# Kernel tuning notes

Measured on AMD Instinct MI355X. Metric: run time of the kernel, lower is better.

Reference implementation:

```python
import jax, jax.numpy as jnp
import numpy as np
from jax import lax

B, T, C, H, W, SV = 1, 12, 10, 256, 256, 3
LAMBDA = 0.05
ITERS = 10


def _to_c(x):
    return lax.complex(x[..., 0], x[..., 1])


def _to_r(x):
    return jnp.stack([jnp.real(x), jnp.imag(x)], axis=-1)


def fft_2d_img(x):
    # torch: fftshift(ifft2(ifftshift(x)))  (backward-norm ifft, same as numpy/jax)
    ax = (-2, -1)
    return jnp.fft.fftshift(jnp.fft.ifft2(jnp.fft.ifftshift(x, axes=ax), axes=ax), axes=ax)


def ifft_2d_img(x):
    ax = (-2, -1)
    return jnp.fft.ifftshift(jnp.fft.fft2(jnp.fft.fftshift(x, axes=ax), axes=ax), axes=ax)


def setup_inputs() -> dict:
    key = jax.random.key(0)
    k0, k1, k2, k3, k4 = jax.random.split(key, 5)
    y = jax.random.normal(k0, (B, T, C, H, W, 2), jnp.float32)
    model_out = jax.random.normal(k1, (B, SV, H, W, 2), jnp.float32)
    sens = jax.random.normal(k2, (B, 1, C, H, W, 2), jnp.float32)
    time_basis = jax.random.normal(k3, (B, T, SV, 2), jnp.float32)
    mask = (jax.random.uniform(k4, (B, T, 1, H, W)) > 0.5).astype(jnp.float32)
    return dict(y=y, model_out=model_out, sens=sens, time_basis=time_basis, mask=mask)


def _adjoint(kspace, sens):
    # kspace: [b,t,c,h,w], sens: [b,1,c,h,w] -> [b,t,h,w]
    img = ifft_2d_img(kspace)
    return jnp.sum(jnp.conj(sens) * img, axis=2)


def _forward_model(data, sens, mask):
    # data: [b,t,h,w] -> masked k-space [b,t,c,h,w]
    coil = sens * data[:, :, None, :, :]
    return mask * fft_2d_img(coil)


def _system_R(x, sens, L, mask):
    # x: [b,sv,h,w]; L: [b,t,sv]
    b, sv, h, w = x.shape
    expanded = jnp.einsum('bts,bsp->btp', L, x.reshape(b, sv, h * w)).reshape(b, L.shape[1], h, w)
    masked_k = _forward_model(expanded, sens, mask)
    comb = _adjoint(masked_k, sens)  # [b,t,h,w]
    fin = jnp.einsum('bts,btp->bsp', jnp.conj(L), comb.reshape(b, L.shape[1], h * w))
    return fin.reshape(b, sv, h, w) + LAMBDA * x


def _cg_solve(A, b_vec):
    z = jnp.zeros_like(b_vec)
    r = b_vec
    p = r
    rs = jnp.vdot(r, r)

    def body(i, state):
        z, r, p, rs = state
        Ap = A(p)
        alpha = rs / jnp.vdot(p, Ap)
        z = z + alpha * p
        r = r - alpha * Ap
        rs_new = jnp.vdot(r, r)
        p = r + (rs_new / rs) * p
        return (z, r, p, rs_new)

    z, _, _, _ = lax.fori_loop(0, ITERS, body, (z, r, p, rs))
    return z


def reference(y, model_out, sens, time_basis, mask):
    yc = _to_c(y)            # [b,t,c,h,w] complex64
    sc = _to_c(sens)         # [b,1,c,h,w]
    mo = _to_c(model_out)    # [b,sv,h,w]
    L = _to_c(time_basis)    # [b,t,sv]
    b, t, c, h, w = yc.shape
    sv = L.shape[-1]

    ah_y = _adjoint(yc, sc)  # [b,t,h,w]
    b_vec = jnp.einsum('bts,btp->bsp', jnp.conj(L), ah_y.reshape(b, t, h * w)).reshape(b, sv, h, w)
    b_vec = b_vec + LAMBDA * mo

    A = lambda x: _system_R(x, sc, L, mask)
    z = _cg_solve(A, b_vec)  # [b,sv,h,w] complex
    return _to_r(z)          # [b,sv,h,w,2] float32
```

## Files before the change

### kernel.cpp

```cpp
#include <hip/hip_runtime.h>
#include <math.h>

#define HW 65536
#define NC 10
#define NT 12
#define LAMBDA_F 0.05f
#define PI_F 3.14159265358979323846f
#define SWZ(i) ((i) ^ ((i) >> 4))

__device__ __forceinline__ float2 cadd(float2 a, float2 b){ return make_float2(a.x+b.x, a.y+b.y); }
__device__ __forceinline__ float2 csub(float2 a, float2 b){ return make_float2(a.x-b.x, a.y-b.y); }
__device__ __forceinline__ float2 cmul(float2 a, float2 b){ return make_float2(a.x*b.x-a.y*b.y, a.x*b.y+a.y*b.x); }
__device__ __forceinline__ float2 cmulj(float2 a, float2 b){ return make_float2(a.x*b.x+a.y*b.y, a.x*b.y-a.y*b.x); }
__device__ __forceinline__ float2 cscale(float2 a, float s){ return make_float2(a.x*s, a.y*s); }

template<int SIGN>
__device__ __forceinline__ void radix4_nt(float2& a0, float2& a1, float2& a2, float2& a3){
  float2 t0=cadd(a0,a2), t1=csub(a0,a2), t2=cadd(a1,a3), t3=csub(a1,a3);
  float2 t3r;
  if constexpr (SIGN < 0) t3r = make_float2(t3.y, -t3.x); else t3r = make_float2(-t3.y, t3.x);
  a0=cadd(t0,t2); a1=cadd(t1,t3r); a2=csub(t0,t2); a3=csub(t1,t3r);
}

template<int SIGN>
__device__ __forceinline__ void radix4_tw(float2& a0, float2& a1, float2& a2, float2& a3, float2 w){
  if constexpr (SIGN > 0) w.y = -w.y;
  float2 w2 = cmul(w, w);
  float2 w3 = cmul(w, w2);
  a1 = cmul(a1, w); a2 = cmul(a2, w2); a3 = cmul(a3, w3);
  radix4_nt<SIGN>(a0, a1, a2, a3);
}

__device__ __forceinline__ float2 twf(int e){
  float s, c;
  __sincosf(-2.0f*PI_F*(float)e*(1.0f/256.0f), &s, &c);
  return make_float2(c, s);
}

template<int SIGN>
__device__ __forceinline__ void fft256(float2* b, int j,
                                       float2 wA, float2 wB, float2 wC,
                                       float2& x0, float2& x1, float2& x2, float2& x3){
  radix4_nt<SIGN>(x0,x1,x2,x3);
  b[SWZ(4*j)]=x0; b[SWZ(4*j+1)]=x1; b[SWZ(4*j+2)]=x2; b[SWZ(4*j+3)]=x3;
  x0=b[SWZ(j)]; x1=b[SWZ(j+64)]; x2=b[SWZ(j+128)]; x3=b[SWZ(j+192)];
  radix4_tw<SIGN>(x0,x1,x2,x3, wA);
  { int i=((j>>2)<<4)+(j&3); b[SWZ(i)]=x0; b[SWZ(i+4)]=x1; b[SWZ(i+8)]=x2; b[SWZ(i+12)]=x3; }
  x0=b[SWZ(j)]; x1=b[SWZ(j+64)]; x2=b[SWZ(j+128)]; x3=b[SWZ(j+192)];
  radix4_tw<SIGN>(x0,x1,x2,x3, wB);
  { int i=((j>>4)<<6)+(j&15); b[SWZ(i)]=x0; b[SWZ(i+16)]=x1; b[SWZ(i+32)]=x2; b[SWZ(i+48)]=x3; }
  x0=b[SWZ(j)]; x1=b[SWZ(j+64)]; x2=b[SWZ(j+128)]; x3=b[SWZ(j+192)];
  radix4_tw<SIGN>(x0,x1,x2,x3, wC);
}

template<int SIGN>
__device__ __forceinline__ void fft256x2(float2* bA, float2* bB, int j,
    float2 wA, float2 wB, float2 wC,
    float2& a0, float2& a1, float2& a2, float2& a3,
    float2& b0, float2& b1, float2& b2, float2& b3){
  radix4_nt<SIGN>(a0,a1,a2,a3); radix4_nt<SIGN>(b0,b1,b2,b3);
  bA[SWZ(4*j)]=a0; bA[SWZ(4*j+1)]=a1; bA[SWZ(4*j+2)]=a2; bA[SWZ(4*j+3)]=a3;
  bB[SWZ(4*j)]=b0; bB[SWZ(4*j+1)]=b1; bB[SWZ(4*j+2)]=b2; bB[SWZ(4*j+3)]=b3;
  a0=bA[SWZ(j)]; a1=bA[SWZ(j+64)]; a2=bA[SWZ(j+128)]; a3=bA[SWZ(j+192)];
  b0=bB[SWZ(j)]; b1=bB[SWZ(j+64)]; b2=bB[SWZ(j+128)]; b3=bB[SWZ(j+192)];
  radix4_tw<SIGN>(a0,a1,a2,a3, wA); radix4_tw<SIGN>(b0,b1,b2,b3, wA);
  { int i=((j>>2)<<4)+(j&3);
    bA[SWZ(i)]=a0; bA[SWZ(i+4)]=a1; bA[SWZ(i+8)]=a2; bA[SWZ(i+12)]=a3;
    bB[SWZ(i)]=b0; bB[SWZ(i+4)]=b1; bB[SWZ(i+8)]=b2; bB[SWZ(i+12)]=b3; }
  a0=bA[SWZ(j)]; a1=bA[SWZ(j+64)]; a2=bA[SWZ(j+128)]; a3=bA[SWZ(j+192)];
  b0=bB[SWZ(j)]; b1=bB[SWZ(j+64)]; b2=bB[SWZ(j+128)]; b3=bB[SWZ(j+192)];
  radix4_tw<SIGN>(a0,a1,a2,a3, wB); radix4_tw<SIGN>(b0,b1,b2,b3, wB);
  { int i=((j>>4)<<6)+(j&15);
    bA[SWZ(i)]=a0; bA[SWZ(i+16)]=a1; bA[SWZ(i+32)]=a2; bA[SWZ(i+48)]=a3;
    bB[SWZ(i)]=b0; bB[SWZ(i+16)]=b1; bB[SWZ(i+32)]=b2; bB[SWZ(i+48)]=b3; }
  a0=bA[SWZ(j)]; a1=bA[SWZ(j+64)]; a2=bA[SWZ(j+128)]; a3=bA[SWZ(j+192)];
  b0=bB[SWZ(j)]; b1=bB[SWZ(j+64)]; b2=bB[SWZ(j+128)]; b3=bB[SWZ(j+192)];
  radix4_tw<SIGN>(a0,a1,a2,a3, wC); radix4_tw<SIGN>(b0,b1,b2,b3, wC);
}

__device__ __forceinline__ void cg_chain(const float* __restrict__ scal,
                                         float f0, float f1, float f2, float f3, float f4,
                                         float rs0, int it,
                                         float& a_re, float& a_im, float& beta){
  float rs = rs0; a_re = 0.f; a_im = 0.f; beta = 0.f;
  for (int k = 0; k < it; k++){
    float pr, pi, rr_, ri_, aa;
    if (k == it-1){ pr=f0; pi=f1; rr_=f2; ri_=f3; aa=f4; }
    else { pr=scal[8+8*k+0]; pi=scal[8+8*k+1]; rr_=scal[8+8*k+2];
           ri_=scal[8+8*k+3]; aa=scal[8+8*k+4]; }
    float den = pr*pr + pi*pi;
    a_re =  rs*pr/den;
    a_im = -rs*pi/den;
    float re_ = a_re*rr_ - a_im*ri_;
    float rs_next = rs - 2.0f*re_ + (a_re*a_re + a_im*a_im)*aa;
    beta = rs_next/rs;
    rs = rs_next;
  }
}

__global__ __launch_bounds__(256) void k_setup(const float* __restrict__ mask,
                                               const float2* __restrict__ Lt,
                                               const float2* __restrict__ y,
                                               float* __restrict__ W9,
                                               float2* __restrict__ bufB,
                                               float* __restrict__ scal,
                                               float* __restrict__ part){
  int tid = threadIdx.x;
  int u = blockIdx.x;
  if (u == 0){
    if (tid < 128) scal[tid] = 0.0f;
    for (int i = tid; i < 6144; i += 256) part[i] = 0.0f;
  }
  if (u < 256){
    int kx = u, ky = tid;
    int mx = (kx + 128) & 255, my = (ky + 128) & 255;
    float d0=0.f,d1=0.f,d2=0.f;
    float2 o01=make_float2(0,0), o02=make_float2(0,0), o12=make_float2(0,0);
    for (int t = 0; t < NT; t++){
      float m = mask[t*HW + my*256 + mx];
      float2 l0 = Lt[t*3+0], l1 = Lt[t*3+1], l2 = Lt[t*3+2];
      d0 += m*(l0.x*l0.x + l0.y*l0.y);
      d1 += m*(l1.x*l1.x + l1.y*l1.y);
      d2 += m*(l2.x*l2.x + l2.y*l2.y);
      o01 = cadd(o01, cscale(cmulj(l0,l1), m));
      o02 = cadd(o02, cscale(cmulj(l0,l2), m));
      o12 = cadd(o12, cscale(cmulj(l1,l2), m));
    }
    const float nrm = 1.0f/65536.0f;
    int idx = kx*256 + ky;
    W9[idx]      = d0*nrm;  W9[idx+HW]   = d1*nrm;  W9[idx+2*HW] = d2*nrm;
    W9[idx+3*HW] = o01.x*nrm; W9[idx+4*HW] = o01.y*nrm;
    W9[idx+5*HW] = o02.x*nrm; W9[idx+6*HW] = o02.y*nrm;
    W9[idx+7*HW] = o12.x*nrm; W9[idx+8*HW] = o12.y*nrm;
  } else {
    int idx = (u-256)*256 + tid;
    int c = idx >> 16, pix = idx & (HW-1);
    int xx = pix & 255, yy2 = pix >> 8;
    float sg = ((xx + yy2) & 1) ? -1.0f : 1.0f;
    float2 a0=make_float2(0,0), a1=make_float2(0,0), a2=make_float2(0,0);
    for (int t = 0; t < NT; t++){
      float2 yv = y[((size_t)(t*NC + c))*HW + pix];
      a0 = cadd(a0, cmulj(Lt[t*3+0], yv));
      a1 = cadd(a1, cmulj(Lt[t*3+1], yv));
      a2 = cadd(a2, cmulj(Lt[t*3+2], yv));
    }
    bufB[((size_t)(c*3+0))*HW + pix] = cscale(a0, sg);
    bufB[((size_t)(c*3+1))*HW + pix] = cscale(a1, sg);
    bufB[((size_t)(c*3+2))*HW + pix] = cscale(a2, sg);
  }
}

__global__ __launch_bounds__(512) void k_rows_plain(const float2* __restrict__ src,
                                                    float2* __restrict__ dst){
  __shared__ float2 tile[8][256];
  int tid = threadIdx.x, g = tid >> 6, j = tid & 63;
  float2 wA = twf((j&3)<<4), wB = twf((j&15)<<2), wC = twf(j);
  int pl = blockIdx.y, ri = blockIdx.x;
  int row = ri*8 + g;
  const float2* sr = src + (size_t)pl*HW + row*256;
  float2 x0=sr[j], x1=sr[j+64], x2=sr[j+128], x3=sr[j+192];
  fft256<-1>(tile[g], j, wA,wB,wC, x0,x1,x2,x3);
  tile[g][j]=x0; tile[g][j+64]=x1; tile[g][j+128]=x2; tile[g][j+192]=x3;
  __syncthreads();
  float2* dT = dst + (size_t)pl*HW;
  int yo2 = (tid&3)*2, kxo = tid>>2;
  #pragma unroll
  for (int kb = 0; kb < 2; kb++){
    int kx = kb*128 + kxo;
    float2 a = tile[yo2][kx], b = tile[yo2+1][kx];
    *(float4*)(dT + (size_t)kx*256 + ri*8 + yo2) = make_float4(a.x,a.y,b.x,b.y);
  }
}

__global__ __launch_bounds__(512) void k_cols_plain(const float2* __restrict__ src,
                                                    float2* __restrict__ dst){
  __shared__ float2 tile[8][256];
  int tid = threadIdx.x, g = tid >> 6, j = tid & 63;
  float2 wA = twf((j&3)<<4), wB = twf((j&15)<<2), wC = twf(j);
  int pl = blockIdx.y, kg = blockIdx.x;
  int kx = kg*8 + g;
  const float2* col = src + (size_t)pl*HW + (size_t)kx*256;
  float2 x0=col[j], x1=col[j+64], x2=col[j+128], x3=col[j+192];
  fft256<-1>(tile[g], j, wA,wB,wC, x0,x1,x2,x3);
  tile[g][j]=x0; tile[g][j+64]=x1; tile[g][j+128]=x2; tile[g][j+192]=x3;
  __syncthreads();
  float2* d = dst + (size_t)pl*HW;
  int kxo2 = (tid&3)*2, yy = tid>>2;
  #pragma unroll
  for (int yb = 0; yb < 2; yb++){
    int yc = yb*128 + yy;
    float2 a = tile[kxo2][yc], b = tile[kxo2+1][yc];
    *(float4*)(d + (size_t)yc*256 + kg*8 + kxo2) = make_float4(a.x,a.y,b.x,b.y);
  }
}

__global__ __launch_bounds__(256) void k_compute_b(const float2* __restrict__ A,
                                                   const float2* __restrict__ sens,
                                                   const float2* __restrict__ mo,
                                                   float2* __restrict__ p,
                                                   float2* __restrict__ r,
                                                   float2* __restrict__ z,
                                                   float* __restrict__ part){
  __shared__ float red[4];
  int idx = blockIdx.x*256 + threadIdx.x;
  int s = idx >> 16, pix = idx & (HW-1);
  int xx = pix & 255, yy = pix >> 8;
  float sg = ((xx + yy) & 1) ? -1.0f : 1.0f;
  float2 accv = make_float2(0,0);
  for (int c = 0; c < NC; c++)
    accv = cadd(accv, cmulj(sens[(size_t)c*HW + pix], A[((size_t)(c*3+s))*HW + pix]));
  float2 b = cadd(cscale(accv, sg), cscale(mo[idx], LAMBDA_F));
  p[idx] = b; r[idx] = b; z[idx] = make_float2(0,0);
  float partv = b.x*b.x + b.y*b.y;
  for (int off = 32; off; off >>= 1) partv += __shfl_down(partv, off);
  int j = threadIdx.x & 63, w = threadIdx.x >> 6;
  if (j == 0) red[w] = partv;
  __syncthreads();
  if (threadIdx.x == 0) part[5*1024 + blockIdx.x] = red[0]+red[1]+red[2]+red[3];
}

__global__ __launch_bounds__(256) void k_rows_op(const float2* __restrict__ rprev,
                                                 const float2* __restrict__ pprev,
                                                 const float2* __restrict__ Apb,
                                                 float2* __restrict__ pout,
                                                 float2* __restrict__ rout,
                                                 float2* __restrict__ z,
                                                 const float2* __restrict__ sens,
                                                 float2* __restrict__ dst,
                                                 float* __restrict__ scal,
                                                 const float* __restrict__ part,
                                                 int iter){
  __shared__ float2 tile[8][256];
  __shared__ float red6[4][6];
  int tid = threadIdx.x, g = tid >> 6, j = tid & 63;
  float2 wA = twf((j&3)<<4), wB = twf((j&15)<<2), wC = twf(j);
  int pl = blockIdx.y, ri = blockIdx.x;
  int c = pl/3, sp = pl - 3*c;
  const float2* Sp = sens + (size_t)c*HW;

  float a_re=0.f, a_im=0.f, beta=0.f;
  if (iter > 0){
    float v[6];
    #pragma unroll
    for (int q = 0; q < 6; q++){
      float x = part[q*1024+tid] + part[q*1024+tid+256]
              + part[q*1024+tid+512] + part[q*1024+tid+768];
      for (int off = 32; off; off >>= 1) x += __shfl_down(x, off);
      v[q] = x;
    }
    if (j == 0){
      #pragma unroll
      for (int q = 0; q < 6; q++) red6[g][q] = v[q];
    }
    __syncthreads();
    float f0 = red6[0][0]+red6[1][0]+red6[2][0]+red6[3][0];
    float f1 = red6[0][1]+red6[1][1]+red6[2][1]+red6[3][1];
    float f2 = red6[0][2]+red6[1][2]+red6[2][2]+red6[3][2];
    float f3 = red6[0][3]+red6[1][3]+red6[2][3]+red6[3][3];
    float f4 = red6[0][4]+red6[1][4]+red6[2][4]+red6[3][4];
    float rs0 = (iter == 1) ? (red6[0][5]+red6[1][5]+red6[2][5]+red6[3][5]) : scal[0];
    cg_chain(scal, f0,f1,f2,f3,f4, rs0, iter, a_re, a_im, beta);
    if (blockIdx.x == 0 && blockIdx.y == 0 && tid == 0){
      scal[8+8*(iter-1)+0]=f0; scal[8+8*(iter-1)+1]=f1; scal[8+8*(iter-1)+2]=f2;
      scal[8+8*(iter-1)+3]=f3; scal[8+8*(iter-1)+4]=f4;
      if (iter == 1) scal[0] = rs0;
    }
  }

  int row0 = ri*8 + g*2, row1 = row0 + 1;
  int baseA = row0*256, baseB = row1*256;
  size_t pbA = (size_t)sp*HW + baseA, pbB = (size_t)sp*HW + baseB;
  float2 pvA[4], pvB[4];
  if (iter == 0){
    #pragma unroll
    for (int q = 0; q < 4; q++){
      pvA[q] = pprev[pbA + j + 64*q];
      pvB[q] = pprev[pbB + j + 64*q];
    }
  } else {
    #pragma unroll
    for (int q = 0; q < 4; q++){
      int x = j + 64*q;
      float2 peA = pprev[pbA+x], reA = rprev[pbA+x], aeA = Apb[pbA+x];
      float2 peB = pprev[pbB+x], reB = rprev[pbB+x], aeB = Apb[pbB+x];
      float2 rnA = make_float2(reA.x - (a_re*aeA.x - a_im*aeA.y),
                               reA.y - (a_re*aeA.y + a_im*aeA.x));
      float2 rnB = make_float2(reB.x - (a_re*aeB.x - a_im*aeB.y),
                               reB.y - (a_re*aeB.y + a_im*aeB.x));
      pvA[q] = make_float2(rnA.x + beta*peA.x, rnA.y + beta*peA.y);
      pvB[q] = make_float2(rnB.x + beta*peB.x, rnB.y + beta*peB.y);
      if (c == 0){
        rout[pbA+x] = rnA;  rout[pbB+x] = rnB;
        pout[pbA+x] = pvA[q]; pout[pbB+x] = pvB[q];
        float2 zA = z[pbA+x], zB = z[pbB+x];
        z[pbA+x] = make_float2(zA.x + a_re*peA.x - a_im*peA.y,
                               zA.y + a_re*peA.y + a_im*peA.x);
        z[pbB+x] = make_float2(zB.x + a_re*peB.x - a_im*peB.y,
                               zB.y + a_re*peB.y + a_im*peB.x);
      }
    }
  }
  float2 xA0 = cmul(Sp[baseA+j],     pvA[0]);
  float2 xA1 = cmul(Sp[baseA+j+64],  pvA[1]);
  float2 xA2 = cmul(Sp[baseA+j+128], pvA[2]);
  float2 xA3 = cmul(Sp[baseA+j+192], pvA[3]);
  float2 xB0 = cmul(Sp[baseB+j],     pvB[0]);
  float2 xB1 = cmul(Sp[baseB+j+64],  pvB[1]);
  float2 xB2 = cmul(Sp[baseB+j+128], pvB[2]);
  float2 xB3 = cmul(Sp[baseB+j+192], pvB[3]);
  fft256x2<1>(tile[g*2], tile[g*2+1], j, wA,wB,wC, xA0,xA1,xA2,xA3, xB0,xB1,xB2,xB3);
  tile[g*2][j]=xA0; tile[g*2][j+64]=xA1; tile[g*2][j+128]=xA2; tile[g*2][j+192]=xA3;
  tile[g*2+1][j]=xB0; tile[g*2+1][j+64]=xB1; tile[g*2+1][j+128]=xB2; tile[g*2+1][j+192]=xB3;
  __syncthreads();
  float2* dT = dst + (size_t)pl*HW;
  int yo2 = (tid&3)*2, kxo = tid>>2;
  #pragma unroll
  for (int kb = 0; kb < 4; kb++){
    int kx = kb*64 + kxo;
    float2 a = tile[yo2][kx], b = tile[yo2+1][kx];
    *(float4*)(dT + (size_t)kx*256 + ri*8 + yo2) = make_float4(a.x,a.y,b.x,b.y);
  }
}

__global__ __launch_bounds__(384) void k_cols_W(const float2* __restrict__ src,
                                                float2* __restrict__ dst,
                                                const float* __restrict__ W9){
  __shared__ float2 tile[12][256];
  int tid = threadIdx.x, w = tid >> 6, j = tid & 63;
  float2 wA = twf((j&3)<<4), wB = twf((j&15)<<2), wC = twf(j);
  int kg = blockIdx.x, c = blockIdx.y;
  int s = w >> 1, kxp = w & 1;
  int kxl0 = kxp*2, kxl1 = kxl0+1;
  int kx0 = kg*4 + kxl0, kx1 = kg*4 + kxl1;
  {
    const float2* colA = src + ((size_t)(c*3+s))*HW + (size_t)kx0*256;
    const float2* colB = src + ((size_t)(c*3+s))*HW + (size_t)kx1*256;
    float2 a0=colA[j], a1=colA[j+64], a2=colA[j+128], a3=colA[j+192];
    float2 b0=colB[j], b1=colB[j+64], b2=colB[j+128], b3=colB[j+192];
    fft256x2<1>(tile[s*4+kxl0], tile[s*4+kxl1], j, wA,wB,wC, a0,a1,a2,a3, b0,b1,b2,b3);
    tile[s*4+kxl0][j]=a0; tile[s*4+kxl0][j+64]=a1; tile[s*4+kxl0][j+128]=a2; tile[s*4+kxl0][j+192]=a3;
    tile[s*4+kxl1][j]=b0; tile[s*4+kxl1][j+64]=b1; tile[s*4+kxl1][j+128]=b2; tile[s*4+kxl1][j+192]=b3;
  }
  __syncthreads();
  float2 UA[4], UB[4];
  #pragma unroll
  for (int q = 0; q < 4; q++){
    int k = j + 64*q;
    {
      int wi = kx0*256 + k;
      float2 v0 = tile[0+kxl0][k], v1 = tile[4+kxl0][k], v2 = tile[8+kxl0][k];
      if (s == 0){
        float d0 = W9[wi];
        float2 o01 = make_float2(W9[wi+3*HW], W9[wi+4*HW]);
        float2 o02 = make_float2(W9[wi+5*HW], W9[wi+6*HW]);
        UA[q] = cadd(cadd(cscale(v0,d0), cmul(o01,v1)), cmul(o02,v2));
      } else if (s == 1){
        float d1 = W9[wi+HW];
        float2 o01 = make_float2(W9[wi+3*HW], W9[wi+4*HW]);
        float2 o12 = make_float2(W9[wi+7*HW], W9[wi+8*HW]);
        UA[q] = cadd(cadd(cmulj(o01,v0), cscale(v1,d1)), cmul(o12,v2));
      } else {
        float d2 = W9[wi+2*HW];
        float2 o02 = make_float2(W9[wi+5*HW], W9[wi+6*HW]);
        float2 o12 = make_float2(W9[wi+7*HW], W9[wi+8*HW]);
        UA[q] = cadd(cadd(cmulj(o02,v0), cmulj(o12,v1)), cscale(v2,d2));
      }
    }
    {
      int wi = kx1*256 + k;
      float2 v0 = tile[0+kxl1][k], v1 = tile[4+kxl1][k], v2 = tile[8+kxl1][k];
      if (s == 0){
        float d0 = W9[wi];
        float2 o01 = make_float2(W9[wi+3*HW], W9[wi+4*HW]);
        float2 o02 = make_float2(W9[wi+5*HW], W9[wi+6*HW]);
        UB[q] = cadd(cadd(cscale(v0,d0), cmul(o01,v1)), cmul(o02,v2));
      } else if (s == 1){
        float d1 = W9[wi+HW];
        float2 o01 = make_float2(W9[wi+3*HW], W9[wi+4*HW]);
        float2 o12 = make_float2(W9[wi+7*HW], W9[wi+8*HW]);
        UB[q] = cadd(cadd(cmulj(o01,v0), cscale(v1,d1)), cmul(o12,v2));
      } else {
        float d2 = W9[wi+2*HW];
        float2 o02 = make_float2(W9[wi+5*HW], W9[wi+6*HW]);
        float2 o12 = make_float2(W9[wi+7*HW], W9[wi+8*HW]);
        UB[q] = cadd(cadd(cmulj(o02,v0), cmulj(o12,v1)), cscale(v2,d2));
      }
    }
  }
  __syncthreads();
  {
    float2 a0=UA[0], a1=UA[1], a2=UA[2], a3=UA[3];
    float2 b0=UB[0], b1=UB[1], b2=UB[2], b3=UB[3];
    fft256x2<-1>(tile[s*4+kxl0], tile[s*4+kxl1], j, wA,wB,wC, a0,a1,a2,a3, b0,b1,b2,b3);
    tile[s*4+kxl0][j]=a0; tile[s*4+kxl0][j+64]=a1; tile[s*4+kxl0][j+128]=a2; tile[s*4+kxl0][j+192]=a3;
    tile[s*4+kxl1][j]=b0; tile[s*4+kxl1][j+64]=b1; tile[s*4+kxl1][j+128]=b2; tile[s*4+kxl1][j+192]=b3;
  }
  __syncthreads();
  #pragma unroll
  for (int yb = 0; yb < 4; yb++){
    int flat = yb*384 + tid;
    int s_out = flat >> 9;
    int rem = flat & 511;
    int kxo2 = (rem >> 8) << 1;
    int yc = rem & 255;
    float2 a = tile[s_out*4+kxo2][yc], b = tile[s_out*4+kxo2+1][yc];
    float2* d = dst + ((size_t)(c*3+s_out))*HW;
    *(float4*)(d + (size_t)yc*256 + kg*4 + kxo2) = make_float4(a.x,a.y,b.x,b.y);
  }
}

__global__ __launch_bounds__(320) void k_rows_acc(const float2* __restrict__ Bp,
                                                  const float2* __restrict__ sens,
                                                  const float2* __restrict__ p,
                                                  const float2* __restrict__ r,
                                                  float2* __restrict__ Ap,
                                                  float* __restrict__ part){
  __shared__ float2 scratch[10][256];
  __shared__ float red5[4][5];
  int tid = threadIdx.x, w = tid >> 6, j = tid & 63;
  float2 wA = twf((j&3)<<4), wB = twf((j&15)<<2), wC = twf(j);
  int row = blockIdx.x, s = blockIdx.y;
  {
    int c0 = 2*w, c1 = 2*w+1;
    const float2* srcA = Bp + ((size_t)(c0*3+s))*HW + row*256;
    const float2* srcB = Bp + ((size_t)(c1*3+s))*HW + row*256;
    float2 a0=srcA[j], a1=srcA[j+64], a2=srcA[j+128], a3=srcA[j+192];
    float2 b0=srcB[j], b1=srcB[j+64], b2=srcB[j+128], b3=srcB[j+192];
    fft256x2<-1>(scratch[c0], scratch[c1], j, wA,wB,wC, a0,a1,a2,a3, b0,b1,b2,b3);
    const float2* ScA = sens + (size_t)c0*HW + row*256;
    const float2* ScB = sens + (size_t)c1*HW + row*256;
    scratch[c0][j]     = cmulj(ScA[j],     a0);
    scratch[c0][j+64]  = cmulj(ScA[j+64],  a1);
    scratch[c0][j+128] = cmulj(ScA[j+128], a2);
    scratch[c0][j+192] = cmulj(ScA[j+192], a3);
    scratch[c1][j]     = cmulj(ScB[j],     b0);
    scratch[c1][j+64]  = cmulj(ScB[j+64],  b1);
    scratch[c1][j+128] = cmulj(ScB[j+128], b2);
    scratch[c1][j+192] = cmulj(ScB[j+192], b3);
  }
  __syncthreads();
  if (tid < 256){
    int k = tid;
    float2 a = make_float2(0,0);
    #pragma unroll
    for (int c = 0; c < NC; c++) a = cadd(a, scratch[c][k]);
    size_t ob = (size_t)s*HW + row*256 + k;
    float2 pv = p[ob];
    float2 ap = cadd(a, cscale(pv, LAMBDA_F));
    Ap[ob] = ap;
    float2 rv = r[ob];
    float s0 = pv.x*ap.x + pv.y*ap.y;
    float s1 = pv.x*ap.y - pv.y*ap.x;
    float s2 = rv.x*ap.x + rv.y*ap.y;
    float s3 = rv.x*ap.y - rv.y*ap.x;
    float s4 = ap.x*ap.x + ap.y*ap.y;
    for (int off = 32; off; off >>= 1){
      s0 += __shfl_down(s0, off); s1 += __shfl_down(s1, off);
      s2 += __shfl_down(s2, off); s3 += __shfl_down(s3, off);
      s4 += __shfl_down(s4, off);
    }
    if (j == 0){ red5[w][0]=s0; red5[w][1]=s1; red5[w][2]=s2; red5[w][3]=s3; red5[w][4]=s4; }
  }
  __syncthreads();
  if (tid == 0){
    int bflat = blockIdx.y*256 + blockIdx.x;
    #pragma unroll
    for (int q = 0; q < 5; q++)
      part[q*1024 + bflat] = red5[0][q]+red5[1][q]+red5[2][q]+red5[3][q];
  }
}

__global__ __launch_bounds__(256) void k_zfin(float2* __restrict__ z,
                                              const float2* __restrict__ p9,
                                              const float* __restrict__ scal,
                                              const float* __restrict__ part){
  __shared__ float red5[4][5];
  int tid = threadIdx.x, g = tid >> 6, j = tid & 63;
  float v[5];
  #pragma unroll
  for (int q = 0; q < 5; q++){
    float x = part[q*1024+tid] + part[q*1024+tid+256]
            + part[q*1024+tid+512] + part[q*1024+tid+768];
    for (int off = 32; off; off >>= 1) x += __shfl_down(x, off);
    v[q] = x;
  }
  if (j == 0){
    #pragma unroll
    for (int q = 0; q < 5; q++) red5[g][q] = v[q];
  }
  __syncthreads();
  float f0 = red5[0][0]+red5[1][0]+red5[2][0]+red5[3][0];
  float f1 = red5[0][1]+red5[1][1]+red5[2][1]+red5[3][1];
  float f2 = red5[0][2]+red5[1][2]+red5[2][2]+red5[3][2];
  float f3 = red5[0][3]+red5[1][3]+red5[2][3]+red5[3][3];
  float f4 = red5[0][4]+red5[1][4]+red5[2][4]+red5[3][4];
  float a_re, a_im, beta;
  cg_chain(scal, f0,f1,f2,f3,f4, scal[0], 10, a_re, a_im, beta);
  int idx = blockIdx.x*256 + tid;
  float2 pe = p9[idx], ze = z[idx];
  z[idx] = make_float2(ze.x + a_re*pe.x - a_im*pe.y,
                       ze.y + a_re*pe.y + a_im*pe.x);
}

extern "C" void kernel_launch(void* const* d_in, const int* in_sizes, int n_in,
                              void* d_out, int out_size, void* d_ws, size_t ws_size,
                              hipStream_t stream){
  const float2* y    = (const float2*)d_in[0];
  const float2* mo   = (const float2*)d_in[1];
  const float2* sens = (const float2*)d_in[2];
  const float2* Lt   = (const float2*)d_in[3];
  const float*  mask = (const float*)d_in[4];

  float* w = (float*)d_ws;
  float*  scal = w;
  float*  part = w + 128;
  float*  W9   = w + 128 + 6144;
  float2* bufA = (float2*)(W9 + 9*HW);
  float2* bufB = bufA + (size_t)30*HW;
  float2* p0   = bufB + (size_t)30*HW;
  float2* p1   = p0 + (size_t)3*HW;
  float2* r0   = p1 + (size_t)3*HW;
  float2* r1   = r0 + (size_t)3*HW;
  float2* Ap   = r1 + (size_t)3*HW;
  float2* z    = (float2*)d_out;

  k_setup<<<2816, 256, 0, stream>>>(mask, Lt, y, W9, bufB, scal, part);
  k_rows_plain<<<dim3(32, 30), 512, 0, stream>>>(bufB, bufA);
  k_cols_plain<<<dim3(32, 30), 512, 0, stream>>>(bufA, bufB);
  k_compute_b<<<768, 256, 0, stream>>>(bufB, sens, mo, p0, r0, z, part);

  for (int it = 0; it < 10; it++){
    float2* pprev = (it == 0) ? p0 : ((it & 1) ? p0 : p1);
    float2* rprev = (it == 0) ? r0 : ((it & 1) ? r0 : r1);
    float2* pw = (it & 1) ? p1 : p0;
    float2* rw = (it & 1) ? r1 : r0;
    k_rows_op<<<dim3(32, 30), 256, 0, stream>>>(rprev, pprev, Ap, pw, rw, z, sens, bufA, scal, part, it);
    k_cols_W<<<dim3(64, 10), 384, 0, stream>>>(bufA, bufB, W9);
    k_rows_acc<<<dim3(256, 3), 320, 0, stream>>>(bufB, sens, pw, rw, Ap, part);
  }
  k_zfin<<<768, 256, 0, stream>>>(z, p1, scal, part);
}
```

Measured before the change: 474.1 us.

## Restructure CG loop into two kernels per iteration using linearity of forward FFT

Reworks each CG iteration from three kernels into two. The column FFT of the search direction p is built from the FFT of r plus beta times the previous k-space direction (Kp), so only r needs a forward row FFT. The row adjoint FFT, coil sum, CG update and forward row FFT of the new residual are fused into one 640-thread kernel. The pAp inner product is computed in the k-space weighting stage, and alpha comes from a recurrence over the stored rs history. This cuts launches and a full pass over the 30-plane buffers per iteration, at the cost of an extra 30-plane Kp buffer that is read and written each iteration, and a different floating-point summation order.

After: 645.0 us. 36.1% more time.

```diff
diff --git a/kernel.cpp b/kernel.cpp
--- a/kernel.cpp
+++ b/kernel.cpp
@@ -7,6 +7,9 @@
 #define LAMBDA_F 0.05f
 #define PI_F 3.14159265358979323846f
 #define SWZ(i) ((i) ^ ((i) >> 4))
+#define ROW_RS(it)  (it)
+#define ROW_PAR(it) (16 + 2*(it))
+#define NPART_ROWS 36
 
 __device__ __forceinline__ float2 cadd(float2 a, float2 b){ return make_float2(a.x+b.x, a.y+b.y); }
 __device__ __forceinline__ float2 csub(float2 a, float2 b){ return make_float2(a.x-b.x, a.y-b.y); }
@@ -78,24 +81,22 @@
   radix4_tw<SIGN>(a0,a1,a2,a3, wC); radix4_tw<SIGN>(b0,b1,b2,b3, wC);
 }
 
-__device__ __forceinline__ void cg_chain(const float* __restrict__ scal,
-                                         float f0, float f1, float f2, float f3, float f4,
-                                         float rs0, int it,
-                                         float& a_re, float& a_im, float& beta){
-  float rs = rs0; a_re = 0.f; a_im = 0.f; beta = 0.f;
-  for (int k = 0; k < it; k++){
-    float pr, pi, rr_, ri_, aa;
-    if (k == it-1){ pr=f0; pi=f1; rr_=f2; ri_=f3; aa=f4; }
-    else { pr=scal[8+8*k+0]; pi=scal[8+8*k+1]; rr_=scal[8+8*k+2];
-           ri_=scal[8+8*k+3]; aa=scal[8+8*k+4]; }
-    float den = pr*pr + pi*pi;
-    a_re =  rs*pr/den;
-    a_im = -rs*pi/den;
-    float re_ = a_re*rr_ - a_im*ri_;
-    float rs_next = rs - 2.0f*re_ + (a_re*a_re + a_im*a_im)*aa;
-    beta = rs_next/rs;
-    rs = rs_next;
-  }
+__device__ __forceinline__ void cg_chain2(const float* __restrict__ scal, int n,
+                                          float parR, float parI,
+                                          float& a_re, float& a_im, float& beta){
+  float rs0 = scal[0];
+  float P2 = rs0, rs_km1 = rs0;
+  beta = 0.f;
+  for (int k = 1; k < n; k++){
+    float rsk = scal[k];
+    beta = rsk / rs_km1;
+    P2 = rsk + beta*beta*P2;
+    rs_km1 = rsk;
+  }
+  float pr = parR + LAMBDA_F*P2, pi = parI;
+  float den = pr*pr + pi*pi;
+  a_re =  rs_km1*pr/den;
+  a_im = -rs_km1*pi/den;
 }
 
 __global__ __launch_bounds__(256) void k_setup(const float* __restrict__ mask,
@@ -109,7 +110,7 @@
   int u = blockIdx.x;
   if (u == 0){
     if (tid < 128) scal[tid] = 0.0f;
-    for (int i = tid; i < 6144; i += 256) part[i] = 0.0f;
+    for (int i = tid; i < NPART_ROWS*1024; i += 256) part[i] = 0.0f;
   }
   if (u < 256){
     int kx = u, ky = tid;
@@ -197,7 +198,6 @@
 __global__ __launch_bounds__(256) void k_compute_b(const float2* __restrict__ A,
                                                    const float2* __restrict__ sens,
                                                    const float2* __restrict__ mo,
-                                                   float2* __restrict__ p,
                                                    float2* __restrict__ r,
                                                    float2* __restrict__ z,
                                                    float* __restrict__ part){
@@ -210,192 +210,257 @@
   for (int c = 0; c < NC; c++)
     accv = cadd(accv, cmulj(sens[(size_t)c*HW + pix], A[((size_t)(c*3+s))*HW + pix]));
   float2 b = cadd(cscale(accv, sg), cscale(mo[idx], LAMBDA_F));
-  p[idx] = b; r[idx] = b; z[idx] = make_float2(0,0);
+  r[idx] = b; z[idx] = make_float2(0,0);
   float partv = b.x*b.x + b.y*b.y;
   for (int off = 32; off; off >>= 1) partv += __shfl_down(partv, off);
   int j = threadIdx.x & 63, w = threadIdx.x >> 6;
   if (j == 0) red[w] = partv;
   __syncthreads();
-  if (threadIdx.x == 0) part[5*1024 + blockIdx.x] = red[0]+red[1]+red[2]+red[3];
-}
-
-__global__ __launch_bounds__(256) void k_rows_op(const float2* __restrict__ rprev,
-                                                 const float2* __restrict__ pprev,
-                                                 const float2* __restrict__ Apb,
-                                                 float2* __restrict__ pout,
-                                                 float2* __restrict__ rout,
-                                                 float2* __restrict__ z,
-                                                 const float2* __restrict__ sens,
-                                                 float2* __restrict__ dst,
-                                                 float* __restrict__ scal,
-                                                 const float* __restrict__ part,
-                                                 int iter){
-  __shared__ float2 tile[8][256];
-  __shared__ float red6[4][6];
-  int tid = threadIdx.x, g = tid >> 6, j = tid & 63;
+  if (threadIdx.x == 0) part[ROW_RS(0)*1024 + blockIdx.x] = red[0]+red[1]+red[2]+red[3];
+}
+
+template<int MODE>
+__global__ __launch_bounds__(640) void k_bigrow(const float2* __restrict__ bufB,
+                                                const float2* __restrict__ sens,
+                                                float2* __restrict__ rbuf,
+                                                float2* __restrict__ pbuf,
+                                                float2* __restrict__ zbuf,
+                                                float2* __restrict__ bufR,
+                                                const float* __restrict__ scal,
+                                                float* __restrict__ part, int iter){
+  __shared__ float2 scratch[10][256];
+  __shared__ float2 rnew_s[256];
+  __shared__ float redv[10];
+  __shared__ float sA[2];
+  int tid = threadIdx.x, w = tid >> 6, j = tid & 63;
   float2 wA = twf((j&3)<<4), wB = twf((j&15)<<2), wC = twf(j);
-  int pl = blockIdx.y, ri = blockIdx.x;
-  int c = pl/3, sp = pl - 3*c;
-  const float2* Sp = sens + (size_t)c*HW;
-
-  float a_re=0.f, a_im=0.f, beta=0.f;
-  if (iter > 0){
-    float v[6];
+  int row = blockIdx.x, s = blockIdx.y;
+
+  if constexpr (MODE == 1){
     #pragma unroll
-    for (int q = 0; q < 6; q++){
-      float x = part[q*1024+tid] + part[q*1024+tid+256]
-              + part[q*1024+tid+512] + part[q*1024+tid+768];
-      for (int off = 32; off; off >>= 1) x += __shfl_down(x, off);
-      v[q] = x;
-    }
-    if (j == 0){
+    for (int q = 0; q < 2; q++){
+      const float* P = part + (ROW_PAR(iter-1)+q)*1024;
+      float v = P[tid] + ((tid < 384) ? P[tid+640] : 0.f);
+      for (int off = 32; off; off >>= 1) v += __shfl_down(v, off);
+      if (j == 0) redv[w] = v;
+      __syncthreads();
+      if (tid == 0){
+        float t = 0.f;
+        #pragma unroll
+        for (int k = 0; k < 10; k++) t += redv[k];
+        sA[q] = t;
+      }
+      __syncthreads();
+    }
+    float a_re, a_im, beta;
+    cg_chain2(scal, iter, sA[0], sA[1], a_re, a_im, beta);
+
+    {
+      int c = w;
+      const float2* src = bufB + ((size_t)(c*3+s))*HW + row*256;
+      float2 x0=src[j], x1=src[j+64], x2=src[j+128], x3=src[j+192];
+      fft256<-1>(scratch[c], j, wA,wB,wC, x0,x1,x2,x3);
+      const float2* Sc = sens + (size_t)c*HW + row*256;
+      scratch[c][j]     = cmulj(Sc[j],     x0);
+      scratch[c][j+64]  = cmulj(Sc[j+64],  x1);
+      scratch[c][j+128] = cmulj(Sc[j+128], x2);
+      scratch[c][j+192] = cmulj(Sc[j+192], x3);
+    }
+    __syncthreads();
+    if (tid < 256){
+      int k = tid;
+      float2 M = make_float2(0,0);
       #pragma unroll
-      for (int q = 0; q < 6; q++) red6[g][q] = v[q];
-    }
-    __syncthreads();
-    float f0 = red6[0][0]+red6[1][0]+red6[2][0]+red6[3][0];
-    float f1 = red6[0][1]+red6[1][1]+red6[2][1]+red6[3][1];
-    float f2 = red6[0][2]+red6[1][2]+red6[2][2]+red6[3][2];
-    float f3 = red6[0][3]+red6[1][3]+red6[2][3]+red6[3][3];
-    float f4 = red6[0][4]+red6[1][4]+red6[2][4]+red6[3][4];
-    float rs0 = (iter == 1) ? (red6[0][5]+red6[1][5]+red6[2][5]+red6[3][5]) : scal[0];
-    cg_chain(scal, f0,f1,f2,f3,f4, rs0, iter, a_re, a_im, beta);
-    if (blockIdx.x == 0 && blockIdx.y == 0 && tid == 0){
-      scal[8+8*(iter-1)+0]=f0; scal[8+8*(iter-1)+1]=f1; scal[8+8*(iter-1)+2]=f2;
-      scal[8+8*(iter-1)+3]=f3; scal[8+8*(iter-1)+4]=f4;
-      if (iter == 1) scal[0] = rs0;
-    }
-  }
-
-  int row0 = ri*8 + g*2, row1 = row0 + 1;
-  int baseA = row0*256, baseB = row1*256;
-  size_t pbA = (size_t)sp*HW + baseA, pbB = (size_t)sp*HW + baseB;
-  float2 pvA[4], pvB[4];
-  if (iter == 0){
-    #pragma unroll
-    for (int q = 0; q < 4; q++){
-      pvA[q] = pprev[pbA + j + 64*q];
-      pvB[q] = pprev[pbB + j + 64*q];
-    }
+      for (int c = 0; c < NC; c++) M = cadd(M, scratch[c][k]);
+      size_t ob = (size_t)s*HW + row*256 + k;
+      float2 rold = rbuf[ob];
+      float2 pcur;
+      if (iter == 1) pcur = rold;
+      else { float2 pold = pbuf[ob]; pcur = cadd(rold, cscale(pold, beta)); }
+      float2 Ap = cadd(M, cscale(pcur, LAMBDA_F));
+      float2 rnew = make_float2(rold.x - (a_re*Ap.x - a_im*Ap.y),
+                                rold.y - (a_re*Ap.y + a_im*Ap.x));
+      float2 zo = zbuf[ob];
+      zbuf[ob] = make_float2(zo.x + a_re*pcur.x - a_im*pcur.y,
+                             zo.y + a_re*pcur.y + a_im*pcur.x);
+      pbuf[ob] = pcur;
+      rbuf[ob] = rnew;
+      rnew_s[k] = rnew;
+      float pv2 = rnew.x*rnew.x + rnew.y*rnew.y;
+      for (int off = 32; off; off >>= 1) pv2 += __shfl_down(pv2, off);
+      if (j == 0) redv[w] = pv2;
+    }
+    __syncthreads();
+    if (tid == 0)
+      part[ROW_RS(iter)*1024 + s*256 + row] = redv[0]+redv[1]+redv[2]+redv[3];
   } else {
-    #pragma unroll
-    for (int q = 0; q < 4; q++){
-      int x = j + 64*q;
-      float2 peA = pprev[pbA+x], reA = rprev[pbA+x], aeA = Apb[pbA+x];
-      float2 peB = pprev[pbB+x], reB = rprev[pbB+x], aeB = Apb[pbB+x];
-      float2 rnA = make_float2(reA.x - (a_re*aeA.x - a_im*aeA.y),
-                               reA.y - (a_re*aeA.y + a_im*aeA.x));
-      float2 rnB = make_float2(reB.x - (a_re*aeB.x - a_im*aeB.y),
-                               reB.y - (a_re*aeB.y + a_im*aeB.x));
-      pvA[q] = make_float2(rnA.x + beta*peA.x, rnA.y + beta*peA.y);
-      pvB[q] = make_float2(rnB.x + beta*peB.x, rnB.y + beta*peB.y);
-      if (c == 0){
-        rout[pbA+x] = rnA;  rout[pbB+x] = rnB;
-        pout[pbA+x] = pvA[q]; pout[pbB+x] = pvB[q];
-        float2 zA = z[pbA+x], zB = z[pbB+x];
-        z[pbA+x] = make_float2(zA.x + a_re*peA.x - a_im*peA.y,
-                               zA.y + a_re*peA.y + a_im*peA.x);
-        z[pbB+x] = make_float2(zB.x + a_re*peB.x - a_im*peB.y,
-                               zB.y + a_re*peB.y + a_im*peB.x);
-      }
-    }
-  }
-  float2 xA0 = cmul(Sp[baseA+j],     pvA[0]);
-  float2 xA1 = cmul(Sp[baseA+j+64],  pvA[1]);
-  float2 xA2 = cmul(Sp[baseA+j+128], pvA[2]);
-  float2 xA3 = cmul(Sp[baseA+j+192], pvA[3]);
-  float2 xB0 = cmul(Sp[baseB+j],     pvB[0]);
-  float2 xB1 = cmul(Sp[baseB+j+64],  pvB[1]);
-  float2 xB2 = cmul(Sp[baseB+j+128], pvB[2]);
-  float2 xB3 = cmul(Sp[baseB+j+192], pvB[3]);
-  fft256x2<1>(tile[g*2], tile[g*2+1], j, wA,wB,wC, xA0,xA1,xA2,xA3, xB0,xB1,xB2,xB3);
-  tile[g*2][j]=xA0; tile[g*2][j+64]=xA1; tile[g*2][j+128]=xA2; tile[g*2][j+192]=xA3;
-  tile[g*2+1][j]=xB0; tile[g*2+1][j+64]=xB1; tile[g*2+1][j+128]=xB2; tile[g*2+1][j+192]=xB3;
-  __syncthreads();
-  float2* dT = dst + (size_t)pl*HW;
-  int yo2 = (tid&3)*2, kxo = tid>>2;
-  #pragma unroll
-  for (int kb = 0; kb < 4; kb++){
-    int kx = kb*64 + kxo;
-    float2 a = tile[yo2][kx], b = tile[yo2+1][kx];
-    *(float4*)(dT + (size_t)kx*256 + ri*8 + yo2) = make_float4(a.x,a.y,b.x,b.y);
-  }
-}
-
-__global__ __launch_bounds__(384) void k_cols_W(const float2* __restrict__ src,
-                                                float2* __restrict__ dst,
-                                                const float* __restrict__ W9){
-  __shared__ float2 tile[12][256];
+    if (tid < 256){
+      size_t ob = (size_t)s*HW + row*256 + tid;
+      rnew_s[tid] = rbuf[ob];
+    }
+    __syncthreads();
+  }
+
+  {
+    int c = w;
+    const float2* Sc = sens + (size_t)c*HW + row*256;
+    float2 x0 = cmul(Sc[j],     rnew_s[j]);
+    float2 x1 = cmul(Sc[j+64],  rnew_s[j+64]);
+    float2 x2 = cmul(Sc[j+128], rnew_s[j+128]);
+    float2 x3 = cmul(Sc[j+192], rnew_s[j+192]);
+    fft256<1>(scratch[c], j, wA,wB,wC, x0,x1,x2,x3);
+    float2* d = bufR + ((size_t)(c*3+s))*HW + row*256;
+    d[j]=x0; d[j+64]=x1; d[j+128]=x2; d[j+192]=x3;
+  }
+}
+
+__global__ __launch_bounds__(384) void k_colW(const float2* __restrict__ bufR,
+                                              float2* __restrict__ Kp,
+                                              float2* __restrict__ bufB,
+                                              const float* __restrict__ W9,
+                                              float* __restrict__ scal,
+                                              float* __restrict__ part, int iter){
+  __shared__ float2 T[12][256];
+  __shared__ float redv[6][2];
+  __shared__ float sB[1];
   int tid = threadIdx.x, w = tid >> 6, j = tid & 63;
   float2 wA = twf((j&3)<<4), wB = twf((j&15)<<2), wC = twf(j);
   int kg = blockIdx.x, c = blockIdx.y;
   int s = w >> 1, kxp = w & 1;
-  int kxl0 = kxp*2, kxl1 = kxl0+1;
+  int kxl0 = kxp*2, kxl1 = kxl0 + 1;
   int kx0 = kg*4 + kxl0, kx1 = kg*4 + kxl1;
+
+  float rs_it;
   {
-    const float2* colA = src + ((size_t)(c*3+s))*HW + (size_t)kx0*256;
-    const float2* colB = src + ((size_t)(c*3+s))*HW + (size_t)kx1*256;
-    float2 a0=colA[j], a1=colA[j+64], a2=colA[j+128], a3=colA[j+192];
-    float2 b0=colB[j], b1=colB[j+64], b2=colB[j+128], b3=colB[j+192];
-    fft256x2<1>(tile[s*4+kxl0], tile[s*4+kxl1], j, wA,wB,wC, a0,a1,a2,a3, b0,b1,b2,b3);
-    tile[s*4+kxl0][j]=a0; tile[s*4+kxl0][j+64]=a1; tile[s*4+kxl0][j+128]=a2; tile[s*4+kxl0][j+192]=a3;
-    tile[s*4+kxl1][j]=b0; tile[s*4+kxl1][j+64]=b1; tile[s*4+kxl1][j+128]=b2; tile[s*4+kxl1][j+192]=b3;
-  }
-  __syncthreads();
+    const float* P = part + ROW_RS(iter)*1024;
+    float v = P[tid] + P[tid+384] + ((tid < 256) ? P[tid+768] : 0.f);
+    for (int off = 32; off; off >>= 1) v += __shfl_down(v, off);
+    if (j == 0) redv[w][0] = v;
+    __syncthreads();
+    if (tid == 0){
+      float t = 0.f;
+      #pragma unroll
+      for (int k = 0; k < 6; k++) t += redv[k][0];
+      sB[0] = t;
+    }
+    __syncthreads();
+    rs_it = sB[0];
+  }
+  float beta = (iter == 0) ? 0.f : rs_it / scal[iter-1];
+  if (blockIdx.x == 0 && blockIdx.y == 0 && tid == 0) scal[iter] = rs_it;
+
+  #pragma unroll
+  for (int f = 0; f < 4; f++){
+    int idx = f*384 + tid;
+    int sp = idx >> 9, rem = idx & 511, rrow = rem >> 1, cp = rem & 1;
+    const float4* s4 = (const float4*)(bufR + ((size_t)(c*3+sp))*HW);
+    float4 v = s4[(size_t)rrow*128 + kg*2 + cp];
+    T[sp*4 + cp*2 + 0][rrow] = make_float2(v.x, v.y);
+    T[sp*4 + cp*2 + 1][rrow] = make_float2(v.z, v.w);
+  }
+  __syncthreads();
+
+  float2 a0=T[s*4+kxl0][j], a1=T[s*4+kxl0][j+64], a2=T[s*4+kxl0][j+128], a3=T[s*4+kxl0][j+192];
+  float2 b0=T[s*4+kxl1][j], b1=T[s*4+kxl1][j+64], b2=T[s*4+kxl1][j+128], b3=T[s*4+kxl1][j+192];
+  fft256x2<1>(T[s*4+kxl0], T[s*4+kxl1], j, wA,wB,wC, a0,a1,a2,a3, b0,b1,b2,b3);
+
+  float2* kpA = Kp + ((size_t)(c*3+s))*HW + (size_t)kx0*256;
+  float2* kpB = Kp + ((size_t)(c*3+s))*HW + (size_t)kx1*256;
+  if (iter > 0){
+    a0 = cadd(a0, cscale(kpA[j],     beta));
+    a1 = cadd(a1, cscale(kpA[j+64],  beta));
+    a2 = cadd(a2, cscale(kpA[j+128], beta));
+    a3 = cadd(a3, cscale(kpA[j+192], beta));
+    b0 = cadd(b0, cscale(kpB[j],     beta));
+    b1 = cadd(b1, cscale(kpB[j+64],  beta));
+    b2 = cadd(b2, cscale(kpB[j+128], beta));
+    b3 = cadd(b3, cscale(kpB[j+192], beta));
+  }
+  kpA[j]=a0; kpA[j+64]=a1; kpA[j+128]=a2; kpA[j+192]=a3;
+  kpB[j]=b0; kpB[j+64]=b1; kpB[j+128]=b2; kpB[j+192]=b3;
+  T[s*4+kxl0][j]=a0; T[s*4+kxl0][j+64]=a1; T[s*4+kxl0][j+128]=a2; T[s*4+kxl0][j+192]=a3;
+  T[s*4+kxl1][j]=b0; T[s*4+kxl1][j+64]=b1; T[s*4+kxl1][j+128]=b2; T[s*4+kxl1][j+192]=b3;
+  __syncthreads();
+
   float2 UA[4], UB[4];
+  float pr = 0.f, pim = 0.f;
   #pragma unroll
   for (int q = 0; q < 4; q++){
     int k = j + 64*q;
     {
       int wi = kx0*256 + k;
-      float2 v0 = tile[0+kxl0][k], v1 = tile[4+kxl0][k], v2 = tile[8+kxl0][k];
+      float2 v0 = T[0+kxl0][k], v1 = T[4+kxl0][k], v2 = T[8+kxl0][k];
+      float2 U;
       if (s == 0){
         float d0 = W9[wi];
         float2 o01 = make_float2(W9[wi+3*HW], W9[wi+4*HW]);
         float2 o02 = make_float2(W9[wi+5*HW], W9[wi+6*HW]);
-        UA[q] = cadd(cadd(cscale(v0,d0), cmul(o01,v1)), cmul(o02,v2));
+        U = cadd(cadd(cscale(v0,d0), cmul(o01,v1)), cmul(o02,v2));
       } else if (s == 1){
         float d1 = W9[wi+HW];
         float2 o01 = make_float2(W9[wi+3*HW], W9[wi+4*HW]);
         float2 o12 = make_float2(W9[wi+7*HW], W9[wi+8*HW]);
-        UA[q] = cadd(cadd(cmulj(o01,v0), cscale(v1,d1)), cmul(o12,v2));
+        U = cadd(cadd(cmulj(o01,v0), cscale(v1,d1)), cmul(o12,v2));
       } else {
         float d2 = W9[wi+2*HW];
         float2 o02 = make_float2(W9[wi+5*HW], W9[wi+6*HW]);
         float2 o12 = make_float2(W9[wi+7*HW], W9[wi+8*HW]);
-        UA[q] = cadd(cadd(cmulj(o02,v0), cmulj(o12,v1)), cscale(v2,d2));
+        U = cadd(cadd(cmulj(o02,v0), cmulj(o12,v1)), cscale(v2,d2));
       }
+      UA[q] = U;
+      float2 vs = (s==0) ? v0 : ((s==1) ? v1 : v2);
+      pr  += vs.x*U.x + vs.y*U.y;
+      pim += vs.x*U.y - vs.y*U.x;
     }
     {
       int wi = kx1*256 + k;
-      float2 v0 = tile[0+kxl1][k], v1 = tile[4+kxl1][k], v2 = tile[8+kxl1][k];
+      float2 v0 = T[0+kxl1][k], v1 = T[4+kxl1][k], v2 = T[8+kxl1][k];
+      float2 U;
       if (s == 0){
         float d0 = W9[wi];
         float2 o01 = make_float2(W9[wi+3*HW], W9[wi+4*HW]);
         float2 o02 = make_float2(W9[wi+5*HW], W9[wi+6*HW]);
-        UB[q] = cadd(cadd(cscale(v0,d0), cmul(o01,v1)), cmul(o02,v2));
+        U = cadd(cadd(cscale(v0,d0), cmul(o01,v1)), cmul(o02,v2));
       } else if (s == 1){
         float d1 = W9[wi+HW];
         float2 o01 = make_float2(W9[wi+3*HW], W9[wi+4*HW]);
         float2 o12 = make_float2(W9[wi+7*HW], W9[wi+8*HW]);
-        UB[q] = cadd(cadd(cmulj(o01,v0), cscale(v1,d1)), cmul(o12,v2));
+        U = cadd(cadd(cmulj(o01,v0), cscale(v1,d1)), cmul(o12,v2));
       } else {
         float d2 = W9[wi+2*HW];
         float2 o02 = make_float2(W9[wi+5*HW], W9[wi+6*HW]);
         float2 o12 = make_float2(W9[wi+7*HW], W9[wi+8*HW]);
-        UB[q] = cadd(cadd(cmulj(o02,v0), cmulj(o12,v1)), cscale(v2,d2));
+        U = cadd(cadd(cmulj(o02,v0), cmulj(o12,v1)), cscale(v2,d2));
       }
-    }
-  }
-  __syncthreads();
+      UB[q] = U;
+      float2 vs = (s==0) ? v0 : ((s==1) ? v1 : v2);
+      pr  += vs.x*U.x + vs.y*U.y;
+      pim += vs.x*U.y - vs.y*U.x;
+    }
+  }
+  __syncthreads();
+
   {
-    float2 a0=UA[0], a1=UA[1], a2=UA[2], a3=UA[3];
-    float2 b0=UB[0], b1=UB[1], b2=UB[2], b3=UB[3];
-    fft256x2<-1>(tile[s*4+kxl0], tile[s*4+kxl1], j, wA,wB,wC, a0,a1,a2,a3, b0,b1,b2,b3);
-    tile[s*4+kxl0][j]=a0; tile[s*4+kxl0][j+64]=a1; tile[s*4+kxl0][j+128]=a2; tile[s*4+kxl0][j+192]=a3;
-    tile[s*4+kxl1][j]=b0; tile[s*4+kxl1][j+64]=b1; tile[s*4+kxl1][j+128]=b2; tile[s*4+kxl1][j+192]=b3;
-  }
-  __syncthreads();
+    float2 c0=UA[0], c1=UA[1], c2=UA[2], c3=UA[3];
+    float2 d0=UB[0], d1=UB[1], d2=UB[2], d3=UB[3];
+    fft256x2<-1>(T[s*4+kxl0], T[s*4+kxl1], j, wA,wB,wC, c0,c1,c2,c3, d0,d1,d2,d3);
+    T[s*4+kxl0][j]=c0; T[s*4+kxl0][j+64]=c1; T[s*4+kxl0][j+128]=c2; T[s*4+kxl0][j+192]=c3;
+    T[s*4+kxl1][j]=d0; T[s*4+kxl1][j+64]=d1; T[s*4+kxl1][j+128]=d2; T[s*4+kxl1][j+192]=d3;
+  }
+  for (int off = 32; off; off >>= 1){
+    pr  += __shfl_down(pr, off);
+    pim += __shfl_down(pim, off);
+  }
+  if (j == 0){ redv[w][0] = pr; redv[w][1] = pim; }
+  __syncthreads();
+  if (tid == 0){
+    float tr = 0.f, ti = 0.f;
+    #pragma unroll
+    for (int k = 0; k < 6; k++){ tr += redv[k][0]; ti += redv[k][1]; }
+    int bflat = c*64 + kg;
+    part[ ROW_PAR(iter)   *1024 + bflat] = tr;
+    part[(ROW_PAR(iter)+1)*1024 + bflat] = ti;
+  }
   #pragma unroll
   for (int yb = 0; yb < 4; yb++){
     int flat = yb*384 + tid;
@@ -403,103 +468,38 @@
     int rem = flat & 511;
     int kxo2 = (rem >> 8) << 1;
     int yc = rem & 255;
-    float2 a = tile[s_out*4+kxo2][yc], b = tile[s_out*4+kxo2+1][yc];
-    float2* d = dst + ((size_t)(c*3+s_out))*HW;
+    float2 a = T[s_out*4+kxo2][yc], b = T[s_out*4+kxo2+1][yc];
+    float2* d = bufB + ((size_t)(c*3+s_out))*HW;
     *(float4*)(d + (size_t)yc*256 + kg*4 + kxo2) = make_float4(a.x,a.y,b.x,b.y);
   }
 }
 
-__global__ __launch_bounds__(320) void k_rows_acc(const float2* __restrict__ Bp,
-                                                  const float2* __restrict__ sens,
-                                                  const float2* __restrict__ p,
-                                                  const float2* __restrict__ r,
-                                                  float2* __restrict__ Ap,
-                                                  float* __restrict__ part){
-  __shared__ float2 scratch[10][256];
-  __shared__ float red5[4][5];
+__global__ __launch_bounds__(256) void k_final(float2* __restrict__ z,
+                                               const float2* __restrict__ rbuf,
+                                               const float2* __restrict__ pbuf,
+                                               const float* __restrict__ scal,
+                                               const float* __restrict__ part){
+  __shared__ float redv[4];
+  __shared__ float sA[2];
   int tid = threadIdx.x, w = tid >> 6, j = tid & 63;
-  float2 wA = twf((j&3)<<4), wB = twf((j&15)<<2), wC = twf(j);
-  int row = blockIdx.x, s = blockIdx.y;
-  {
-    int c0 = 2*w, c1 = 2*w+1;
-    const float2* srcA = Bp + ((size_t)(c0*3+s))*HW + row*256;
-    const float2* srcB = Bp + ((size_t)(c1*3+s))*HW + row*256;
-    float2 a0=srcA[j], a1=srcA[j+64], a2=srcA[j+128], a3=srcA[j+192];
-    float2 b0=srcB[j], b1=srcB[j+64], b2=srcB[j+128], b3=srcB[j+192];
-    fft256x2<-1>(scratch[c0], scratch[c1], j, wA,wB,wC, a0,a1,a2,a3, b0,b1,b2,b3);
-    const float2* ScA = sens + (size_t)c0*HW + row*256;
-    const float2* ScB = sens + (size_t)c1*HW + row*256;
-    scratch[c0][j]     = cmulj(ScA[j],     a0);
-    scratch[c0][j+64]  = cmulj(ScA[j+64],  a1);
-    scratch[c0][j+128] = cmulj(ScA[j+128], a2);
-    scratch[c0][j+192] = cmulj(ScA[j+192], a3);
-    scratch[c1][j]     = cmulj(ScB[j],     b0);
-    scratch[c1][j+64]  = cmulj(ScB[j+64],  b1);
-    scratch[c1][j+128] = cmulj(ScB[j+128], b2);
-    scratch[c1][j+192] = cmulj(ScB[j+192], b3);
-  }
-  __syncthreads();
-  if (tid < 256){
-    int k = tid;
-    float2 a = make_float2(0,0);
-    #pragma unroll
-    for (int c = 0; c < NC; c++) a = cadd(a, scratch[c][k]);
-    size_t ob = (size_t)s*HW + row*256 + k;
-    float2 pv = p[ob];
-    float2 ap = cadd(a, cscale(pv, LAMBDA_F));
-    Ap[ob] = ap;
-    float2 rv = r[ob];
-    float s0 = pv.x*ap.x + pv.y*ap.y;
-    float s1 = pv.x*ap.y - pv.y*ap.x;
-    float s2 = rv.x*ap.x + rv.y*ap.y;
-    float s3 = rv.x*ap.y - rv.y*ap.x;
-    float s4 = ap.x*ap.x + ap.y*ap.y;
-    for (int off = 32; off; off >>= 1){
-      s0 += __shfl_down(s0, off); s1 += __shfl_down(s1, off);
-      s2 += __shfl_down(s2, off); s3 += __shfl_down(s3, off);
-      s4 += __shfl_down(s4, off);
-    }
-    if (j == 0){ red5[w][0]=s0; red5[w][1]=s1; red5[w][2]=s2; red5[w][3]=s3; red5[w][4]=s4; }
-  }
-  __syncthreads();
-  if (tid == 0){
-    int bflat = blockIdx.y*256 + blockIdx.x;
-    #pragma unroll
-    for (int q = 0; q < 5; q++)
-      part[q*1024 + bflat] = red5[0][q]+red5[1][q]+red5[2][q]+red5[3][q];
-  }
-}
-
-__global__ __launch_bounds__(256) void k_zfin(float2* __restrict__ z,
-                                              const float2* __restrict__ p9,
-                                              const float* __restrict__ scal,
-                                              const float* __restrict__ part){
-  __shared__ float red5[4][5];
-  int tid = threadIdx.x, g = tid >> 6, j = tid & 63;
-  float v[5];
   #pragma unroll
-  for (int q = 0; q < 5; q++){
-    float x = part[q*1024+tid] + part[q*1024+tid+256]
-            + part[q*1024+tid+512] + part[q*1024+tid+768];
-    for (int off = 32; off; off >>= 1) x += __shfl_down(x, off);
-    v[q] = x;
-  }
-  if (j == 0){
-    #pragma unroll
-    for (int q = 0; q < 5; q++) red5[g][q] = v[q];
-  }
-  __syncthreads();
-  float f0 = red5[0][0]+red5[1][0]+red5[2][0]+red5[3][0];
-  float f1 = red5[0][1]+red5[1][1]+red5[2][1]+red5[3][1];
-  float f2 = red5[0][2]+red5[1][2]+red5[2][2]+red5[3][2];
-  float f3 = red5[0][3]+red5[1][3]+red5[2][3]+red5[3][3];
-  float f4 = red5[0][4]+red5[1][4]+red5[2][4]+red5[3][4];
+  for (int q = 0; q < 2; q++){
+    const float* P = part + (ROW_PAR(9)+q)*1024;
+    float v = P[tid] + P[tid+256] + P[tid+512] + P[tid+768];
+    for (int off = 32; off; off >>= 1) v += __shfl_down(v, off);
+    if (j == 0) redv[w] = v;
+    __syncthreads();
+    if (tid == 0) sA[q] = redv[0]+redv[1]+redv[2]+redv[3];
+    __syncthreads();
+  }
   float a_re, a_im, beta;
-  cg_chain(scal, f0,f1,f2,f3,f4, scal[0], 10, a_re, a_im, beta);
+  cg_chain2(scal, 10, sA[0], sA[1], a_re, a_im, beta);
   int idx = blockIdx.x*256 + tid;
-  float2 pe = p9[idx], ze = z[idx];
-  z[idx] = make_float2(ze.x + a_re*pe.x - a_im*pe.y,
-                       ze.y + a_re*pe.y + a_im*pe.x);
+  float2 r9 = rbuf[idx], p8 = pbuf[idx];
+  float2 p9 = cadd(r9, cscale(p8, beta));
+  float2 zo = z[idx];
+  z[idx] = make_float2(zo.x + a_re*p9.x - a_im*p9.y,
+                       zo.y + a_re*p9.y + a_im*p9.x);
 }
 
 extern "C" void kernel_launch(void* const* d_in, const int* in_sizes, int n_in,
@@ -514,29 +514,25 @@
   float* w = (float*)d_ws;
   float*  scal = w;
   float*  part = w + 128;
-  float*  W9   = w + 128 + 6144;
-  float2* bufA = (float2*)(W9 + 9*HW);
-  float2* bufB = bufA + (size_t)30*HW;
-  float2* p0   = bufB + (size_t)30*HW;
-  float2* p1   = p0 + (size_t)3*HW;
-  float2* r0   = p1 + (size_t)3*HW;
-  float2* r1   = r0 + (size_t)3*HW;
-  float2* Ap   = r1 + (size_t)3*HW;
+  float*  W9   = part + NPART_ROWS*1024;
+  float2* bufB = (float2*)(W9 + 9*HW);
+  float2* bufR = bufB + (size_t)30*HW;
+  float2* Kp   = bufR + (size_t)30*HW;
+  float2* rb   = Kp + (size_t)30*HW;
+  float2* pb   = rb + (size_t)3*HW;
   float2* z    = (float2*)d_out;
 
   k_setup<<<2816, 256, 0, stream>>>(mask, Lt, y, W9, bufB, scal, part);
-  k_rows_plain<<<dim3(32, 30), 512, 0, stream>>>(bufB, bufA);
-  k_cols_plain<<<dim3(32, 30), 512, 0, stream>>>(bufA, bufB);
-  k_compute_b<<<768, 256, 0, stream>>>(bufB, sens, mo, p0, r0, z, part);
+  k_rows_plain<<<dim3(32, 30), 512, 0, stream>>>(bufB, bufR);
+  k_cols_plain<<<dim3(32, 30), 512, 0, stream>>>(bufR, bufB);
+  k_compute_b<<<768, 256, 0, stream>>>(bufB, sens, mo, rb, z, part);
+
+  k_bigrow<0><<<dim3(256, 3), 640, 0, stream>>>(bufB, sens, rb, pb, z, bufR, scal, part, 0);
 
   for (int it = 0; it < 10; it++){
-    float2* pprev = (it == 0) ? p0 : ((it & 1) ? p0 : p1);
-    float2* rprev = (it == 0) ? r0 : ((it & 1) ? r0 : r1);
-    float2* pw = (it & 1) ? p1 : p0;
-    float2* rw = (it & 1) ? r1 : r0;
-    k_rows_op<<<dim3(32, 30), 256, 0, stream>>>(rprev, pprev, Ap, pw, rw, z, sens, bufA, scal, part, it);
-    k_cols_W<<<dim3(64, 10), 384, 0, stream>>>(bufA, bufB, W9);
-    k_rows_acc<<<dim3(256, 3), 320, 0, stream>>>(bufB, sens, pw, rw, Ap, part);
-  }
-  k_zfin<<<768, 256, 0, stream>>>(z, p1, scal, part);
-}
+    if (it > 0)
+      k_bigrow<1><<<dim3(256, 3), 640, 0, stream>>>(bufB, sens, rb, pb, z, bufR, scal, part, it);
+    k_colW<<<dim3(64, 10), 384, 0, stream>>>(bufR, Kp, bufB, W9, scal, part, it);
+  }
+  k_final<<<768, 256, 0, stream>>>(z, rb, pb, scal, part);
+}
```
